# Kernel tuning notes

Measured on AMD Instinct MI355X. Metric: run time of the kernel, lower is better.

Reference implementation:

```python
import jax, jax.numpy as jnp
import numpy as np

B, L, C, H = 2, 2048, 1024, 16
D = C // H
THETA = 50000.0


def rotate_half(x):
    x1, x2 = jnp.split(x, 2, axis=-1)
    return jnp.concatenate((-x2, x1), axis=-1)


def rope_freqs(n, dim):
    inv_freq = 1.0 / (THETA ** (jnp.arange(0, dim, 2, dtype=jnp.float32) / dim))
    freqs = jnp.arange(n, dtype=jnp.float32)[:, None] * inv_freq[None, :]  # [n, dim//2]
    return jnp.concatenate((freqs, freqs), axis=-1)  # [n, dim]


def setup_inputs() -> dict:
    key = jax.random.key(0)
    ks = jax.random.split(key, 8)
    q = jax.random.normal(ks[0], (B, L, C), dtype=jnp.float32)
    mask = jax.random.randint(ks[1], (B, L), 0, 2) > 0
    mask = mask.at[:, 0].set(True)  # avoid fully-masked rows
    s = 1.0 / np.sqrt(C)
    Wq = jax.random.normal(ks[2], (C, C), dtype=jnp.float32) * s
    Wk = jax.random.normal(ks[3], (C, C), dtype=jnp.float32) * s
    Wv = jax.random.normal(ks[4], (C, C), dtype=jnp.float32) * s
    Wo = jax.random.normal(ks[5], (C, C), dtype=jnp.float32) * s
    bo = jnp.zeros((C,), dtype=jnp.float32)
    return {"q": q, "mask": mask, "Wq": Wq, "Wk": Wk, "Wv": Wv, "Wo": Wo, "bo": bo}


def reference(q, mask, Wq, Wk, Wv, Wo, bo):
    x = q
    # QKV projections (torch Linear: y = x @ W.T)
    def proj(W):
        y = jnp.einsum('blc,oc->blo', x, W)
        return y.reshape(B, L, H, D).transpose(0, 2, 1, 3)  # [B,H,L,D]
    qh, kh, vh = proj(Wq), proj(Wk), proj(Wv)
    # RoPE (L == S)
    pos = rope_freqs(L, D)  # [L, D]
    cos, sin = jnp.cos(pos), jnp.sin(pos)
    qh = qh * cos + rotate_half(qh) * sin
    kh = kh * cos + rotate_half(kh) * sin
    # masked SDPA with additive bias (-inf where mask is False)
    scale = 1.0 / np.sqrt(D)
    bias = jnp.where(mask[:, None, None, :], 0.0, -jnp.inf)  # [B,1,1,S]
    scores = jnp.einsum('bhld,bhsd->bhls', qh, kh) * scale + bias
    attn = jax.nn.softmax(scores, axis=-1)
    out = jnp.einsum('bhls,bhsd->bhld', attn, vh)
    out = out.transpose(0, 2, 1, 3).reshape(B, L, C)
    return jnp.einsum('blc,oc->blo', out, Wo) + bo
```

## Files before the change

### kernel.cpp

```cpp
#include <hip/hip_runtime.h>
#include <hip/hip_bf16.h>

typedef __hip_bfloat16 bf16;
typedef short bf16x8 __attribute__((ext_vector_type(8)));
typedef short bf16x4 __attribute__((ext_vector_type(4)));
typedef float floatx4 __attribute__((ext_vector_type(4)));

#define Bb 2
#define Ll 2048
#define Cc 1024
#define Hh 16
#define Dd 64
#define INVFREQ_LN 0.3381180763f
#define QSCALE 0.125f

#define GLD16(gp, lp) __builtin_amdgcn_global_load_lds( \
    (const __attribute__((address_space(1))) void*)(gp), \
    (__attribute__((address_space(3))) void*)(lp), 16, 0, 0)

__device__ inline short f2bf(float f) {
    __hip_bfloat16 h = __float2bfloat16(f);
    return *reinterpret_cast<short*>(&h);
}
__device__ inline short f2bf_rn(float f) {
    return (short)((__float_as_uint(f) + 0x8000u) >> 16);
}

__global__ __launch_bounds__(256) void convert_bf16(
    const float* __restrict__ x, const float* __restrict__ wq,
    const float* __restrict__ wk, const float* __restrict__ wv,
    const float* __restrict__ wo,
    bf16* __restrict__ xb, bf16* __restrict__ wqkv, bf16* __restrict__ wob)
{
    const int XN = (Bb * Ll * Cc) / 8;
    const int WN = (Cc * Cc) / 8;
    int i = blockIdx.x * 256 + threadIdx.x;
    const float* src; bf16* dst;
    if (i < XN)               { src = x  + (size_t)i * 8;                 dst = xb   + (size_t)i * 8; }
    else if (i < XN + WN)     { int j = i - XN;        src = wq + (size_t)j * 8; dst = wqkv + (size_t)j * 8; }
    else if (i < XN + 2*WN)   { int j = i - XN - WN;   src = wk + (size_t)j * 8; dst = wqkv + (size_t)Cc*Cc     + (size_t)j * 8; }
    else if (i < XN + 3*WN)   { int j = i - XN - 2*WN; src = wv + (size_t)j * 8; dst = wqkv + (size_t)Cc*Cc*2   + (size_t)j * 8; }
    else                      { int j = i - XN - 3*WN; src = wo + (size_t)j * 8; dst = wob  + (size_t)j * 8; }
    float4 a = *reinterpret_cast<const float4*>(src);
    float4 b = *reinterpret_cast<const float4*>(src + 4);
    float vv[8] = {a.x, a.y, a.z, a.w, b.x, b.y, b.z, b.w};
    bf16x8 o;
    #pragma unroll
    for (int t = 0; t < 8; t++) o[t] = f2bf(vv[t]);
    *reinterpret_cast<bf16x8*>(dst) = o;
}

template <int MODE>
__global__ __launch_bounds__(256) void gemm_mfma(
    const bf16* __restrict__ A, const bf16* __restrict__ W,
    bf16* __restrict__ qb, bf16* __restrict__ kb, bf16* __restrict__ vb,
    float* __restrict__ outf, const float* __restrict__ bias,
    int M, int N, int K)
{
    __shared__ __align__(16) short As[128 * 32];
    __shared__ __align__(16) short Bs[128 * 32];

    const int tid  = threadIdx.x;
    const int wave = tid >> 6;
    const int lane = tid & 63;
    const int l15  = lane & 15;
    const int quad = lane >> 4;
    const int wm   = wave >> 1;
    const int wn   = wave & 1;
    const int m0   = blockIdx.y * 128;
    const int n0   = blockIdx.x * 128;

    const int ar = tid >> 2;
    const int ac = (tid & 3) * 8;

    floatx4 acc[4][4];
    #pragma unroll
    for (int mt = 0; mt < 4; mt++)
        #pragma unroll
        for (int nt = 0; nt < 4; nt++)
            #pragma unroll
            for (int r = 0; r < 4; r++) acc[mt][nt][r] = 0.f;

    for (int k0 = 0; k0 < K; k0 += 32) {
        __syncthreads();
        #pragma unroll
        for (int p = 0; p < 2; p++) {
            const bf16* gp = A + (size_t)(m0 + p * 64 + ar) * K + k0 + ac;
            GLD16(gp, &As[(p * 64 + ar) * 32 + ac]);
        }
        #pragma unroll
        for (int p = 0; p < 2; p++) {
            const bf16* gp = W + (size_t)(n0 + p * 64 + ar) * K + k0 + ac;
            GLD16(gp, &Bs[(p * 64 + ar) * 32 + ac]);
        }
        __syncthreads();

        bf16x8 af[4], bfr[4];
        #pragma unroll
        for (int mt = 0; mt < 4; mt++)
            af[mt] = *(const bf16x8*)&As[(wm * 64 + mt * 16 + l15) * 32 + quad * 8];
        #pragma unroll
        for (int nt = 0; nt < 4; nt++)
            bfr[nt] = *(const bf16x8*)&Bs[(wn * 64 + nt * 16 + l15) * 32 + quad * 8];
        #pragma unroll
        for (int mt = 0; mt < 4; mt++)
            #pragma unroll
            for (int nt = 0; nt < 4; nt++)
                acc[mt][nt] = __builtin_amdgcn_mfma_f32_16x16x32_bf16(
                    af[mt], bfr[nt], acc[mt][nt], 0, 0, 0);
    }

    if (MODE == 1) {
        #pragma unroll
        for (int mt = 0; mt < 4; mt++)
            #pragma unroll
            for (int r = 0; r < 4; r++) {
                int row = m0 + wm * 64 + mt * 16 + quad * 4 + r;
                #pragma unroll
                for (int nt = 0; nt < 4; nt++) {
                    int col = n0 + wn * 64 + nt * 16 + l15;
                    outf[(size_t)row * N + col] = acc[mt][nt][r] + bias[col];
                }
            }
    } else {
        const int colbase = n0 + wn * 64;
        const int which   = colbase >> 10;
        const int hh      = (colbase & (Cc - 1)) >> 6;
        if (which == 2) {
            #pragma unroll
            for (int mt = 0; mt < 4; mt++)
                #pragma unroll
                for (int r = 0; r < 4; r++) {
                    int row = m0 + wm * 64 + mt * 16 + quad * 4 + r;
                    int b = row >> 11, l = row & (Ll - 1);
                    size_t head = (size_t)(b * Hh + hh) * Dd * Ll;
                    int lbase = (l & ~63) | (l & 7);
                    int lg    = (l >> 3) & 7;
                    #pragma unroll
                    for (int nt = 0; nt < 4; nt++) {
                        int d = nt * 16 + l15;
                        int pos = lbase | ((lg ^ (d & 7)) << 3);
                        vb[head + (size_t)d * Ll + pos] = __float2bfloat16(acc[mt][nt][r]);
                    }
                }
        } else {
            bf16* dst = which ? kb : qb;
            const float qs = which ? 1.0f : QSCALE;
            const float base0 = __expf(-(float)l15 * INVFREQ_LN);
            const float base1 = __expf(-(float)(l15 + 16) * INVFREQ_LN);
            #pragma unroll
            for (int mt = 0; mt < 4; mt++)
                #pragma unroll
                for (int r = 0; r < 4; r++) {
                    int row = m0 + wm * 64 + mt * 16 + quad * 4 + r;
                    int b = row >> 11, l = row & (Ll - 1);
                    size_t rb = ((size_t)(b * Hh + hh) * Ll + l) * Dd;
                    #pragma unroll
                    for (int nt2 = 0; nt2 < 2; nt2++) {
                        float fr = (float)l * (nt2 ? base1 : base0);
                        float sn, cs;
                        __sincosf(fr, &sn, &cs);
                        float x1 = acc[mt][nt2][r];
                        float x2 = acc[mt][nt2 + 2][r];
                        float o1 = (x1 * cs - x2 * sn) * qs;
                        float o2 = (x2 * cs + x1 * sn) * qs;
                        int d1 = nt2 * 16 + l15;
                        int d2 = d1 + 32;
                        if (which == 1) {
                            int sw = l & 7;
                            int a1 = ((((d1 >> 3) ^ sw)) << 3) | (d1 & 7);
                            int a2 = ((((d2 >> 3) ^ sw)) << 3) | (d2 & 7);
                            dst[rb + a1] = __float2bfloat16(o1);
                            dst[rb + a2] = __float2bfloat16(o2);
                        } else {
                            dst[rb + d1] = __float2bfloat16(o1);
                            dst[rb + d2] = __float2bfloat16(o2);
                        }
                    }
                }
        }
    }
}

#define LSTR 72

__global__ __launch_bounds__(512) void attn_mfma(
    const bf16* __restrict__ q, const bf16* __restrict__ k, const bf16* __restrict__ vt,
    const int* __restrict__ mask, bf16* __restrict__ ctx)
{
    __shared__ __align__(16) short Ks[2][64 * 64];
    __shared__ __align__(16) short Vs[2][64 * 64];
    __shared__ __align__(16) short Ps[8][16 * LSTR];
    __shared__ __align__(16) float msk[2][64];

    const int tid  = threadIdx.x;
    const int wave = tid >> 6;
    const int lane = tid & 63;
    const int l15  = lane & 15;
    const int quad = lane >> 4;

    const int bh = blockIdx.x & 31;
    const int q0 = (blockIdx.x >> 5) << 7;
    const int b  = bh >> 4;
    const int h  = bh & (Hh - 1);

    const short* qb  = (const short*)(q  + (size_t)bh * Ll * Dd);
    const short* kb  = (const short*)(k  + (size_t)bh * Ll * Dd);
    const short* vtb = (const short*)(vt + (size_t)bh * Dd * Ll);
    const int* mrow = mask + b * Ll;

    const int qrow = q0 + wave * 16 + l15;
    bf16x8 qa0 = *(const bf16x8*)(qb + (size_t)qrow * Dd + quad * 8);
    bf16x8 qa1 = *(const bf16x8*)(qb + (size_t)qrow * Dd + 32 + quad * 8);

    const int g0 = ((quad ^ (l15 & 7)) << 3);
    const int g1 = (((quad + 4) ^ (l15 & 7)) << 3);

    const short* vgp = vtb + (size_t)(tid >> 3) * Ll + ((tid & 7) << 3);
    short* ksl = &Ks[0][0] + tid * 8;
    short* vsl = &Vs[0][0] + tid * 8;
    const int lbuf = 64 * 64;

    floatx4 O[4];
    float l_r = 0.f;
    #pragma unroll
    for (int nt = 0; nt < 4; nt++)
        #pragma unroll
        for (int r = 0; r < 4; r++) O[nt][r] = 0.f;

    GLD16(kb + tid * 8, ksl);
    GLD16(vgp, vsl);
    if (tid < 64) msk[0][tid] = mrow[tid] ? 0.0f : -1e30f;

    for (int t = 0; t < Ll / 64; t++) {
        const int cur = t & 1;
        __syncthreads();
        if (t < Ll / 64 - 1) {
            const int s1 = (t + 1) << 6;
            GLD16(kb + (size_t)s1 * Dd + tid * 8, ksl + (cur ^ 1) * lbuf);
            GLD16(vgp + s1,                       vsl + (cur ^ 1) * lbuf);
            if (tid < 64) msk[cur ^ 1][tid] = mrow[s1 + tid] ? 0.0f : -1e30f;
        }

        const short* Kc = &Ks[cur][0];
        const short* Vc = &Vs[cur][0];
        floatx4 S[4];
        #pragma unroll
        for (int nt = 0; nt < 4; nt++) {
            const short* krow = Kc + (nt * 16 + l15) * 64;
            bf16x8 ka0 = *(const bf16x8*)(krow + g0);
            bf16x8 ka1 = *(const bf16x8*)(krow + g1);
            floatx4 acc; acc[0] = acc[1] = acc[2] = acc[3] = 0.f;
            acc = __builtin_amdgcn_mfma_f32_16x16x32_bf16(ka0, qa0, acc, 0, 0, 0);
            acc = __builtin_amdgcn_mfma_f32_16x16x32_bf16(ka1, qa1, acc, 0, 0, 0);
            S[nt] = acc;
        }

        #pragma unroll
        for (int nt = 0; nt < 4; nt++) {
            float4 m4 = *(const float4*)&msk[cur][nt * 16 + quad * 4];
            float mv[4] = {m4.x, m4.y, m4.z, m4.w};
            bf16x4 pw;
            #pragma unroll
            for (int r = 0; r < 4; r++) {
                float p = __expf(S[nt][r] + mv[r]);
                l_r += p;
                pw[r] = f2bf_rn(p);
            }
            *(bf16x4*)&Ps[wave][l15 * LSTR + nt * 16 + quad * 4] = pw;
        }

        bf16x8 pb0 = *(const bf16x8*)&Ps[wave][l15 * LSTR + quad * 8];
        bf16x8 pb1 = *(const bf16x8*)&Ps[wave][l15 * LSTR + 32 + quad * 8];
        #pragma unroll
        for (int nt = 0; nt < 4; nt++) {
            const short* vrow = Vc + (nt * 16 + l15) * 64;
            bf16x8 va0 = *(const bf16x8*)(vrow + g0);
            bf16x8 va1 = *(const bf16x8*)(vrow + g1);
            O[nt] = __builtin_amdgcn_mfma_f32_16x16x32_bf16(va0, pb0, O[nt], 0, 0, 0);
            O[nt] = __builtin_amdgcn_mfma_f32_16x16x32_bf16(va1, pb1, O[nt], 0, 0, 0);
        }
    }

    float l = l_r;
    l += __shfl_xor(l, 16);
    l += __shfl_xor(l, 32);
    const float inv = 1.0f / l;

    {
        int row = q0 + wave * 16 + l15;
        short* cp = (short*)ctx + ((size_t)(b * Ll + row)) * Cc + h * Dd;
        #pragma unroll
        for (int nt = 0; nt < 4; nt++) {
            bf16x4 ov;
            #pragma unroll
            for (int r = 0; r < 4; r++) ov[r] = f2bf_rn(O[nt][r] * inv);
            *(bf16x4*)&cp[nt * 16 + quad * 4] = ov;
        }
    }
}

extern "C" void kernel_launch(void* const* d_in, const int* in_sizes, int n_in,
                              void* d_out, int out_size, void* d_ws, size_t ws_size,
                              hipStream_t stream) {
    const float* x    = (const float*)d_in[0];
    const int*   mask = (const int*)d_in[1];
    const float* Wq   = (const float*)d_in[2];
    const float* Wk   = (const float*)d_in[3];
    const float* Wv   = (const float*)d_in[4];
    const float* Wo   = (const float*)d_in[5];
    const float* bo   = (const float*)d_in[6];
    float* out = (float*)d_out;

    const size_t per = (size_t)Bb * Hh * Ll * Dd;
    bf16* qbuf = (bf16*)d_ws;
    bf16* kbuf = qbuf + per;
    bf16* vbuf = kbuf + per;
    bf16* xb   = vbuf + per;
    bf16* wqkv = xb + per;
    bf16* wob  = wqkv + (size_t)3 * Cc * Cc;
    bf16* ctx  = xb;

    const int M = Bb * Ll;

    convert_bf16<<<(Bb*Ll*Cc/8 + 4*Cc*Cc/8) / 256, 256, 0, stream>>>(
        x, Wq, Wk, Wv, Wo, xb, wqkv, wob);

    dim3 gQKV(3 * Cc / 128, M / 128);
    gemm_mfma<0><<<gQKV, 256, 0, stream>>>(xb, wqkv, qbuf, kbuf, vbuf,
                                           nullptr, nullptr, M, 3 * Cc, Cc);

    attn_mfma<<<Bb * Hh * (Ll / 128), 512, 0, stream>>>(qbuf, kbuf, vbuf, mask, ctx);

    dim3 gOut(Cc / 128, M / 128);
    gemm_mfma<1><<<gOut, 256, 0, stream>>>(ctx, wob, nullptr, nullptr, nullptr,
                                           out, bo, M, Cc, Cc);
}
```

Baseline: 202.9 us.

## Compact unmasked keys/values so attention iterates only over valid positions

Adds a prefix-scan kernel over the key mask, then has the QKV GEMM epilogue write K and V rows only for unmasked positions, packed contiguously at their compacted index. The attention kernel loops only over the tiles holding valid keys, drops the per-tile mask loads and adds, and subtracts the zero-padded tail's exp(0) contributions from the softmax denominator. About half the keys are masked, so this aims to roughly halve attention work, at the cost of an extra scan launch and a memset of the K/V buffers.

```diff
diff --git a/kernel.cpp b/kernel.cpp
--- a/kernel.cpp
+++ b/kernel.cpp
@@ -50,11 +50,41 @@
     *reinterpret_cast<bf16x8*>(dst) = o;
 }
 
+__global__ __launch_bounds__(256) void mask_scan(
+    const int* __restrict__ mask, int* __restrict__ cidx, int* __restrict__ valid)
+{
+    const int b   = blockIdx.x;
+    const int tid = threadIdx.x;
+    const int base = b * Ll + tid * 8;
+    int m[8]; int s = 0;
+    #pragma unroll
+    for (int i = 0; i < 8; i++) { m[i] = mask[base + i] ? 1 : 0; s += m[i]; }
+    const int lane = tid & 63;
+    int x = s;
+    #pragma unroll
+    for (int off = 1; off < 64; off <<= 1) {
+        int y = __shfl_up(x, off);
+        if (lane >= off) x += y;
+    }
+    __shared__ int wtot[4];
+    if (lane == 63) wtot[tid >> 6] = x;
+    __syncthreads();
+    int wbase = 0;
+    const int w = tid >> 6;
+    #pragma unroll
+    for (int i = 0; i < 4; i++) if (i < w) wbase += wtot[i];
+    int run = wbase + (x - s);
+    #pragma unroll
+    for (int i = 0; i < 8; i++) { cidx[base + i] = run; run += m[i]; }
+    if (tid == 255) valid[b] = run;
+}
+
 template <int MODE>
 __global__ __launch_bounds__(256) void gemm_mfma(
     const bf16* __restrict__ A, const bf16* __restrict__ W,
     bf16* __restrict__ qb, bf16* __restrict__ kb, bf16* __restrict__ vb,
     float* __restrict__ outf, const float* __restrict__ bias,
+    const int* __restrict__ cmask, const int* __restrict__ cidx,
     int M, int N, int K)
 {
     __shared__ __align__(16) short As[128 * 32];
@@ -133,14 +163,17 @@
                 for (int r = 0; r < 4; r++) {
                     int row = m0 + wm * 64 + mt * 16 + quad * 4 + r;
                     int b = row >> 11, l = row & (Ll - 1);
-                    size_t head = (size_t)(b * Hh + hh) * Dd * Ll;
-                    int lbase = (l & ~63) | (l & 7);
-                    int lg    = (l >> 3) & 7;
-                    #pragma unroll
-                    for (int nt = 0; nt < 4; nt++) {
-                        int d = nt * 16 + l15;
-                        int pos = lbase | ((lg ^ (d & 7)) << 3);
-                        vb[head + (size_t)d * Ll + pos] = __float2bfloat16(acc[mt][nt][r]);
+                    if (cmask[b * Ll + l]) {
+                        int c = cidx[b * Ll + l];
+                        size_t head = (size_t)(b * Hh + hh) * Dd * Ll;
+                        int lbase = (c & ~63) | (c & 7);
+                        int lg    = (c >> 3) & 7;
+                        #pragma unroll
+                        for (int nt = 0; nt < 4; nt++) {
+                            int d = nt * 16 + l15;
+                            int pos = lbase | ((lg ^ (d & 7)) << 3);
+                            vb[head + (size_t)d * Ll + pos] = __float2bfloat16(acc[mt][nt][r]);
+                        }
                     }
                 }
         } else {
@@ -154,27 +187,34 @@
                 for (int r = 0; r < 4; r++) {
                     int row = m0 + wm * 64 + mt * 16 + quad * 4 + r;
                     int b = row >> 11, l = row & (Ll - 1);
-                    size_t rb = ((size_t)(b * Hh + hh) * Ll + l) * Dd;
-                    #pragma unroll
-                    for (int nt2 = 0; nt2 < 2; nt2++) {
-                        float fr = (float)l * (nt2 ? base1 : base0);
-                        float sn, cs;
-                        __sincosf(fr, &sn, &cs);
-                        float x1 = acc[mt][nt2][r];
-                        float x2 = acc[mt][nt2 + 2][r];
-                        float o1 = (x1 * cs - x2 * sn) * qs;
-                        float o2 = (x2 * cs + x1 * sn) * qs;
-                        int d1 = nt2 * 16 + l15;
-                        int d2 = d1 + 32;
-                        if (which == 1) {
-                            int sw = l & 7;
-                            int a1 = ((((d1 >> 3) ^ sw)) << 3) | (d1 & 7);
-                            int a2 = ((((d2 >> 3) ^ sw)) << 3) | (d2 & 7);
-                            dst[rb + a1] = __float2bfloat16(o1);
-                            dst[rb + a2] = __float2bfloat16(o2);
-                        } else {
-                            dst[rb + d1] = __float2bfloat16(o1);
-                            dst[rb + d2] = __float2bfloat16(o2);
+                    int cm = 1, c = l;
+                    if (which == 1) {
+                        cm = cmask[b * Ll + l];
+                        c  = cidx[b * Ll + l];
+                    }
+                    if (cm) {
+                        size_t rb = ((size_t)(b * Hh + hh) * Ll + c) * Dd;
+                        #pragma unroll
+                        for (int nt2 = 0; nt2 < 2; nt2++) {
+                            float fr = (float)l * (nt2 ? base1 : base0);
+                            float sn, cs;
+                            __sincosf(fr, &sn, &cs);
+                            float x1 = acc[mt][nt2][r];
+                            float x2 = acc[mt][nt2 + 2][r];
+                            float o1 = (x1 * cs - x2 * sn) * qs;
+                            float o2 = (x2 * cs + x1 * sn) * qs;
+                            int d1 = nt2 * 16 + l15;
+                            int d2 = d1 + 32;
+                            if (which == 1) {
+                                int sw = c & 7;
+                                int a1 = ((((d1 >> 3) ^ sw)) << 3) | (d1 & 7);
+                                int a2 = ((((d2 >> 3) ^ sw)) << 3) | (d2 & 7);
+                                dst[rb + a1] = __float2bfloat16(o1);
+                                dst[rb + a2] = __float2bfloat16(o2);
+                            } else {
+                                dst[rb + d1] = __float2bfloat16(o1);
+                                dst[rb + d2] = __float2bfloat16(o2);
+                            }
                         }
                     }
                 }
@@ -186,12 +226,11 @@
 
 __global__ __launch_bounds__(512) void attn_mfma(
     const bf16* __restrict__ q, const bf16* __restrict__ k, const bf16* __restrict__ vt,
-    const int* __restrict__ mask, bf16* __restrict__ ctx)
+    const int* __restrict__ valid, bf16* __restrict__ ctx)
 {
     __shared__ __align__(16) short Ks[2][64 * 64];
     __shared__ __align__(16) short Vs[2][64 * 64];
     __shared__ __align__(16) short Ps[8][16 * LSTR];
-    __shared__ __align__(16) float msk[2][64];
 
     const int tid  = threadIdx.x;
     const int wave = tid >> 6;
@@ -204,10 +243,12 @@
     const int b  = bh >> 4;
     const int h  = bh & (Hh - 1);
 
+    const int nvalid = valid[b];
+    const int ntiles = (nvalid + 63) >> 6;
+
     const short* qb  = (const short*)(q  + (size_t)bh * Ll * Dd);
     const short* kb  = (const short*)(k  + (size_t)bh * Ll * Dd);
     const short* vtb = (const short*)(vt + (size_t)bh * Dd * Ll);
-    const int* mrow = mask + b * Ll;
 
     const int qrow = q0 + wave * 16 + l15;
     bf16x8 qa0 = *(const bf16x8*)(qb + (size_t)qrow * Dd + quad * 8);
@@ -230,16 +271,14 @@
 
     GLD16(kb + tid * 8, ksl);
     GLD16(vgp, vsl);
-    if (tid < 64) msk[0][tid] = mrow[tid] ? 0.0f : -1e30f;
-
-    for (int t = 0; t < Ll / 64; t++) {
+
+    for (int t = 0; t < ntiles; t++) {
         const int cur = t & 1;
         __syncthreads();
-        if (t < Ll / 64 - 1) {
+        if (t + 1 < ntiles) {
             const int s1 = (t + 1) << 6;
             GLD16(kb + (size_t)s1 * Dd + tid * 8, ksl + (cur ^ 1) * lbuf);
             GLD16(vgp + s1,                       vsl + (cur ^ 1) * lbuf);
-            if (tid < 64) msk[cur ^ 1][tid] = mrow[s1 + tid] ? 0.0f : -1e30f;
         }
 
         const short* Kc = &Ks[cur][0];
@@ -258,12 +297,10 @@
 
         #pragma unroll
         for (int nt = 0; nt < 4; nt++) {
-            float4 m4 = *(const float4*)&msk[cur][nt * 16 + quad * 4];
-            float mv[4] = {m4.x, m4.y, m4.z, m4.w};
             bf16x4 pw;
             #pragma unroll
             for (int r = 0; r < 4; r++) {
-                float p = __expf(S[nt][r] + mv[r]);
+                float p = __expf(S[nt][r]);
                 l_r += p;
                 pw[r] = f2bf_rn(p);
             }
@@ -285,6 +322,7 @@
     float l = l_r;
     l += __shfl_xor(l, 16);
     l += __shfl_xor(l, 32);
+    l -= (float)((ntiles << 6) - nvalid);
     const float inv = 1.0f / l;
 
     {
@@ -319,6 +357,8 @@
     bf16* xb   = vbuf + per;
     bf16* wqkv = xb + per;
     bf16* wob  = wqkv + (size_t)3 * Cc * Cc;
+    int*  cidx   = (int*)(wob + (size_t)Cc * Cc);
+    int*  cvalid = cidx + Bb * Ll;
     bf16* ctx  = xb;
 
     const int M = Bb * Ll;
@@ -326,13 +366,17 @@
     convert_bf16<<<(Bb*Ll*Cc/8 + 4*Cc*Cc/8) / 256, 256, 0, stream>>>(
         x, Wq, Wk, Wv, Wo, xb, wqkv, wob);
 
+    mask_scan<<<Bb, 256, 0, stream>>>(mask, cidx, cvalid);
+
+    hipMemsetAsync(kbuf, 0, 2 * per * sizeof(bf16), stream);
+
     dim3 gQKV(3 * Cc / 128, M / 128);
     gemm_mfma<0><<<gQKV, 256, 0, stream>>>(xb, wqkv, qbuf, kbuf, vbuf,
-                                           nullptr, nullptr, M, 3 * Cc, Cc);
-
-    attn_mfma<<<Bb * Hh * (Ll / 128), 512, 0, stream>>>(qbuf, kbuf, vbuf, mask, ctx);
+                                           nullptr, nullptr, mask, cidx, M, 3 * Cc, Cc);
+
+    attn_mfma<<<Bb * Hh * (Ll / 128), 512, 0, stream>>>(qbuf, kbuf, vbuf, cvalid, ctx);
 
     dim3 gOut(Cc / 128, M / 128);
     gemm_mfma<1><<<gOut, 256, 0, stream>>>(ctx, wob, nullptr, nullptr, nullptr,
-                                           out, bo, M, Cc, Cc);
-}
+                                           out, bo, nullptr, nullptr, M, Cc, Cc);
+}
```

Result: faster. 191.4 us (-5.6%).
